# Optimization experiments

Hardware: AMD Instinct MI355X
Metric: run time of the kernel (lower is better)

## Reference

```python
import jax, jax.numpy as jnp
import numpy as np

LN_EPS = 1e-5

def setup_inputs() -> dict:
    key = jax.random.key(0)
    ks = jax.random.split(key, 6)
    B, H, W, C = 32, 128, 96, 128
    ch = C // 2
    x = jax.random.normal(ks[0], (B, H, W, C), dtype=jnp.float32)
    # he_normal-style scaled init for 1x1 conv kernels (fan_in = C or ch)
    wq_ch = jax.random.normal(ks[1], (C,), dtype=jnp.float32) * np.float32(np.sqrt(2.0 / C))
    wv_ch = jax.random.normal(ks[2], (C, ch), dtype=jnp.float32) * np.float32(np.sqrt(2.0 / C))
    w_ch = jax.random.normal(ks[3], (ch, C), dtype=jnp.float32) * np.float32(np.sqrt(2.0 / ch))
    gamma = jnp.ones((C,), dtype=jnp.float32)
    beta = jnp.zeros((C,), dtype=jnp.float32)
    wq_sp = jax.random.normal(ks[4], (C, ch), dtype=jnp.float32) * np.float32(np.sqrt(2.0 / C))
    wv_sp = jax.random.normal(ks[5], (C, ch), dtype=jnp.float32) * np.float32(np.sqrt(2.0 / C))
    return {"x": x, "wq_ch": wq_ch, "wv_ch": wv_ch, "w_ch": w_ch,
            "gamma": gamma, "beta": beta, "wq_sp": wq_sp, "wv_sp": wv_sp}


def reference(x, wq_ch, wv_ch, w_ch, gamma, beta, wq_sp, wv_sp):
    B, H, W, C = x.shape
    hw = H * W
    ch = C // 2

    # ---- channel-only self-attention ----
    # q: 1x1 conv C->1, flatten to [B, HW], softmax over spatial positions
    q = jnp.einsum('bhwc,c->bhw', x, wq_ch).reshape(B, hw)
    q = jax.nn.softmax(q, axis=-1)
    # v: 1x1 conv C->C/2, flatten to [B, HW, C/2]
    v = jnp.einsum('bhwc,cd->bhwd', x, wv_ch).reshape(B, hw, ch)
    ctx = jnp.einsum('bn,bnd->bd', q, v)          # [B, C/2]
    ctx = ctx @ w_ch                               # 1x1 conv C/2 -> C, [B, C]
    # LayerNorm over axes [1,2,3] of (B,1,1,C) == per-sample norm over C
    mu = jnp.mean(ctx, axis=-1, keepdims=True)
    var = jnp.mean(jnp.square(ctx - mu), axis=-1, keepdims=True)
    ctx = (ctx - mu) * jax.lax.rsqrt(var + LN_EPS) * gamma + beta
    mask_ch = jax.nn.sigmoid(ctx)                  # [B, C]
    ch_out = x * mask_ch[:, None, None, :]

    # ---- spatial-only self-attention (parallel mode: input is x) ----
    # 1x1 conv C->C/2 followed by global avg pool == avg-pooled x projected
    q_sp = jnp.einsum('bhwc,cd->bd', x, wq_sp) / hw  # [B, C/2]
    q_sp = jax.nn.softmax(q_sp, axis=-1)
    v_sp = jnp.einsum('bhwc,cd->bhwd', x, wv_sp).reshape(B, hw, ch)
    sp_ctx = jnp.einsum('bd,bnd->bn', q_sp, v_sp).reshape(B, H, W, 1)
    sp_out = x * jax.nn.sigmoid(sp_ctx)

    return ch_out + sp_out
```

## Files before the change

### kernel.cpp

```cpp
#include <hip/hip_runtime.h>

#define BSZ 32
#define CC  128
#define CH  64
#define HWN 12288
#define BPB 64
#define ROWS (HWN/BPB)

using f4 = __attribute__((ext_vector_type(4))) float;

__global__ __launch_bounds__(256) void psa_pass1(
    const float* __restrict__ x, const float* __restrict__ wq_ch,
    float* __restrict__ pS, float* __restrict__ pX, float* __restrict__ pZ)
{
    const int b    = blockIdx.x / BPB;
    const int blk  = blockIdx.x % BPB;
    const int tid  = threadIdx.x;
    const int l32  = tid & 31;
    const int slot = tid >> 5;

    const f4 wq = reinterpret_cast<const f4*>(wq_ch)[l32];

    float s0=0.f,s1=0.f,s2=0.f,s3=0.f;
    float a0=0.f,a1=0.f,a2=0.f,a3=0.f;
    float zacc=0.f;

    const float* xb = x + (size_t)b * (size_t)(HWN * CC);
    const int row0 = blk * ROWS;

    for (int i = slot; i < ROWS; i += 32) {
        const f4 x0 = reinterpret_cast<const f4*>(xb + (size_t)(row0 + i)      * CC)[l32];
        const f4 x1 = reinterpret_cast<const f4*>(xb + (size_t)(row0 + i + 8)  * CC)[l32];
        const f4 x2 = reinterpret_cast<const f4*>(xb + (size_t)(row0 + i + 16) * CC)[l32];
        const f4 x3 = reinterpret_cast<const f4*>(xb + (size_t)(row0 + i + 24) * CC)[l32];
        float p0 = x0.x*wq.x + x0.y*wq.y + x0.z*wq.z + x0.w*wq.w;
        float p1 = x1.x*wq.x + x1.y*wq.y + x1.z*wq.z + x1.w*wq.w;
        float p2 = x2.x*wq.x + x2.y*wq.y + x2.z*wq.z + x2.w*wq.w;
        float p3 = x3.x*wq.x + x3.y*wq.y + x3.z*wq.z + x3.w*wq.w;
        p0 += __shfl_xor(p0, 1);  p1 += __shfl_xor(p1, 1);
        p2 += __shfl_xor(p2, 1);  p3 += __shfl_xor(p3, 1);
        p0 += __shfl_xor(p0, 2);  p1 += __shfl_xor(p1, 2);
        p2 += __shfl_xor(p2, 2);  p3 += __shfl_xor(p3, 2);
        p0 += __shfl_xor(p0, 4);  p1 += __shfl_xor(p1, 4);
        p2 += __shfl_xor(p2, 4);  p3 += __shfl_xor(p3, 4);
        p0 += __shfl_xor(p0, 8);  p1 += __shfl_xor(p1, 8);
        p2 += __shfl_xor(p2, 8);  p3 += __shfl_xor(p3, 8);
        p0 += __shfl_xor(p0, 16); p1 += __shfl_xor(p1, 16);
        p2 += __shfl_xor(p2, 16); p3 += __shfl_xor(p3, 16);
        const float e0 = __expf(p0), e1 = __expf(p1);
        const float e2 = __expf(p2), e3 = __expf(p3);
        if (l32 == 0) zacc += (e0 + e1) + (e2 + e3);
        s0 += e0*x0.x + e1*x1.x + e2*x2.x + e3*x3.x;
        s1 += e0*x0.y + e1*x1.y + e2*x2.y + e3*x3.y;
        s2 += e0*x0.z + e1*x1.z + e2*x2.z + e3*x3.z;
        s3 += e0*x0.w + e1*x1.w + e2*x2.w + e3*x3.w;
        a0 += (x0.x + x1.x) + (x2.x + x3.x);
        a1 += (x0.y + x1.y) + (x2.y + x3.y);
        a2 += (x0.z + x1.z) + (x2.z + x3.z);
        a3 += (x0.w + x1.w) + (x2.w + x3.w);
    }

    __shared__ float Ssh[CC];
    __shared__ float Xsh[CC];
    __shared__ float zsh;
    if (tid < CC) { Ssh[tid] = 0.f; Xsh[tid] = 0.f; }
    if (tid == 0) zsh = 0.f;
    __syncthreads();

    const int cb = l32 * 4;
    atomicAdd(&Ssh[cb+0], s0); atomicAdd(&Ssh[cb+1], s1);
    atomicAdd(&Ssh[cb+2], s2); atomicAdd(&Ssh[cb+3], s3);
    atomicAdd(&Xsh[cb+0], a0); atomicAdd(&Xsh[cb+1], a1);
    atomicAdd(&Xsh[cb+2], a2); atomicAdd(&Xsh[cb+3], a3);
    if (l32 == 0) atomicAdd(&zsh, zacc);
    __syncthreads();

    const size_t base = (size_t)(b * BPB + blk) * CC;
    if (tid < CC) {
        pS[base + tid] = Ssh[tid];
        pX[base + tid] = Xsh[tid];
    }
    if (tid == 0) pZ[b * BPB + blk] = zsh;
}

__global__ __launch_bounds__(128) void psa_mid(
    const float* __restrict__ pS, const float* __restrict__ pX,
    const float* __restrict__ pZ,
    const float* __restrict__ wv_ch, const float* __restrict__ w_ch,
    const float* __restrict__ gamma, const float* __restrict__ beta,
    const float* __restrict__ wq_sp, const float* __restrict__ wv_sp,
    float* __restrict__ mask_ch, float* __restrict__ wf)
{
    const int b = blockIdx.x;
    const int t = threadIdx.x;

    __shared__ float Ssh[CC], Xsh[CC], ctxh[CH], qsp[CH], zsh, red2[2];

    {
        const float* pSb = pS + (size_t)b * BPB * CC;
        const float* pXb = pX + (size_t)b * BPB * CC;
        float s = 0.f, a = 0.f;
        #pragma unroll
        for (int k = 0; k < BPB; ++k) {
            s += pSb[(size_t)k * CC + t];
            a += pXb[(size_t)k * CC + t];
        }
        Ssh[t] = s; Xsh[t] = a;
    }
    if (t < 64) {
        float z = pZ[b * BPB + t];
        z += __shfl_xor(z, 1); z += __shfl_xor(z, 2);  z += __shfl_xor(z, 4);
        z += __shfl_xor(z, 8); z += __shfl_xor(z, 16); z += __shfl_xor(z, 32);
        if (t == 0) zsh = z;
    }
    __syncthreads();

    if (t < CH) {
        float a = 0.f, aq = 0.f;
        #pragma unroll
        for (int c = 0; c < CC; ++c) {
            a  += Ssh[c] * wv_ch[c*CH + t];
            aq += Xsh[c] * wq_sp[c*CH + t];
        }
        ctxh[t] = a / zsh;
        float q = aq * (1.0f / (float)HWN);
        float m = q;
        m = fmaxf(m, __shfl_xor(m, 1));  m = fmaxf(m, __shfl_xor(m, 2));
        m = fmaxf(m, __shfl_xor(m, 4));  m = fmaxf(m, __shfl_xor(m, 8));
        m = fmaxf(m, __shfl_xor(m, 16)); m = fmaxf(m, __shfl_xor(m, 32));
        float e = __expf(q - m);
        float sum = e;
        sum += __shfl_xor(sum, 1);  sum += __shfl_xor(sum, 2);
        sum += __shfl_xor(sum, 4);  sum += __shfl_xor(sum, 8);
        sum += __shfl_xor(sum, 16); sum += __shfl_xor(sum, 32);
        qsp[t] = e / sum;
    }
    __syncthreads();

    float ctx = 0.f;
    #pragma unroll
    for (int d = 0; d < CH; ++d) ctx += ctxh[d] * w_ch[d*CC + t];

    const int wid = t >> 6;
    {
        float r = ctx;
        r += __shfl_xor(r, 1);  r += __shfl_xor(r, 2);  r += __shfl_xor(r, 4);
        r += __shfl_xor(r, 8);  r += __shfl_xor(r, 16); r += __shfl_xor(r, 32);
        if ((t & 63) == 0) red2[wid] = r;
    }
    __syncthreads();
    const float mu = (red2[0] + red2[1]) * (1.0f / CC);
    __syncthreads();
    const float dc = ctx - mu;
    {
        float r = dc * dc;
        r += __shfl_xor(r, 1);  r += __shfl_xor(r, 2);  r += __shfl_xor(r, 4);
        r += __shfl_xor(r, 8);  r += __shfl_xor(r, 16); r += __shfl_xor(r, 32);
        if ((t & 63) == 0) red2[wid] = r;
    }
    __syncthreads();
    const float var = (red2[0] + red2[1]) * (1.0f / CC);

    const float nrm = dc * rsqrtf(var + 1e-5f) * gamma[t] + beta[t];
    mask_ch[b*CC + t] = 1.0f / (1.0f + __expf(-nrm));

    float wacc = 0.f;
    #pragma unroll
    for (int d = 0; d < CH; ++d) wacc += wv_sp[t*CH + d] * qsp[d];
    wf[b*CC + t] = wacc;
}

__global__ __launch_bounds__(256) void psa_pass2(
    const float* __restrict__ x, const float* __restrict__ mask_ch,
    const float* __restrict__ wf, float* __restrict__ out)
{
    const int b    = blockIdx.x / BPB;
    const int blk  = blockIdx.x % BPB;
    const int tid  = threadIdx.x;
    const int l32  = tid & 31;
    const int slot = tid >> 5;

    const f4 m4 = reinterpret_cast<const f4*>(mask_ch + b*CC)[l32];
    const f4 w4 = reinterpret_cast<const f4*>(wf + b*CC)[l32];

    const float* xb = x   + (size_t)b * (size_t)(HWN * CC);
    float*       ob = out + (size_t)b * (size_t)(HWN * CC);
    const int row0 = blk * ROWS;

    for (int i = slot; i < ROWS; i += 32) {
        const size_t off0 = (size_t)(row0 + i)      * CC;
        const size_t off1 = (size_t)(row0 + i + 8)  * CC;
        const size_t off2 = (size_t)(row0 + i + 16) * CC;
        const size_t off3 = (size_t)(row0 + i + 24) * CC;
        const f4 x0 = reinterpret_cast<const f4*>(xb + off0)[l32];
        const f4 x1 = reinterpret_cast<const f4*>(xb + off1)[l32];
        const f4 x2 = reinterpret_cast<const f4*>(xb + off2)[l32];
        const f4 x3 = reinterpret_cast<const f4*>(xb + off3)[l32];
        float p0 = x0.x*w4.x + x0.y*w4.y + x0.z*w4.z + x0.w*w4.w;
        float p1 = x1.x*w4.x + x1.y*w4.y + x1.z*w4.z + x1.w*w4.w;
        float p2 = x2.x*w4.x + x2.y*w4.y + x2.z*w4.z + x2.w*w4.w;
        float p3 = x3.x*w4.x + x3.y*w4.y + x3.z*w4.z + x3.w*w4.w;
        p0 += __shfl_xor(p0, 1);  p1 += __shfl_xor(p1, 1);
        p2 += __shfl_xor(p2, 1);  p3 += __shfl_xor(p3, 1);
        p0 += __shfl_xor(p0, 2);  p1 += __shfl_xor(p1, 2);
        p2 += __shfl_xor(p2, 2);  p3 += __shfl_xor(p3, 2);
        p0 += __shfl_xor(p0, 4);  p1 += __shfl_xor(p1, 4);
        p2 += __shfl_xor(p2, 4);  p3 += __shfl_xor(p3, 4);
        p0 += __shfl_xor(p0, 8);  p1 += __shfl_xor(p1, 8);
        p2 += __shfl_xor(p2, 8);  p3 += __shfl_xor(p3, 8);
        p0 += __shfl_xor(p0, 16); p1 += __shfl_xor(p1, 16);
        p2 += __shfl_xor(p2, 16); p3 += __shfl_xor(p3, 16);
        const float g0 = 1.0f / (1.0f + __expf(-p0));
        const float g1 = 1.0f / (1.0f + __expf(-p1));
        const float g2 = 1.0f / (1.0f + __expf(-p2));
        const float g3 = 1.0f / (1.0f + __expf(-p3));
        f4 o0, o1, o2, o3;
        o0.x = x0.x*(m4.x+g0); o0.y = x0.y*(m4.y+g0); o0.z = x0.z*(m4.z+g0); o0.w = x0.w*(m4.w+g0);
        o1.x = x1.x*(m4.x+g1); o1.y = x1.y*(m4.y+g1); o1.z = x1.z*(m4.z+g1); o1.w = x1.w*(m4.w+g1);
        o2.x = x2.x*(m4.x+g2); o2.y = x2.y*(m4.y+g2); o2.z = x2.z*(m4.z+g2); o2.w = x2.w*(m4.w+g2);
        o3.x = x3.x*(m4.x+g3); o3.y = x3.y*(m4.y+g3); o3.z = x3.z*(m4.z+g3); o3.w = x3.w*(m4.w+g3);
        __builtin_nontemporal_store(o0, reinterpret_cast<f4*>(ob + off0) + l32);
        __builtin_nontemporal_store(o1, reinterpret_cast<f4*>(ob + off1) + l32);
        __builtin_nontemporal_store(o2, reinterpret_cast<f4*>(ob + off2) + l32);
        __builtin_nontemporal_store(o3, reinterpret_cast<f4*>(ob + off3) + l32);
    }
}

extern "C" void kernel_launch(void* const* d_in, const int* in_sizes, int n_in,
                              void* d_out, int out_size, void* d_ws, size_t ws_size,
                              hipStream_t stream) {
    const float* x     = (const float*)d_in[0];
    const float* wq_ch = (const float*)d_in[1];
    const float* wv_ch = (const float*)d_in[2];
    const float* w_ch  = (const float*)d_in[3];
    const float* gamma = (const float*)d_in[4];
    const float* beta  = (const float*)d_in[5];
    const float* wq_sp = (const float*)d_in[6];
    const float* wv_sp = (const float*)d_in[7];
    float* out = (float*)d_out;

    float* ws   = (float*)d_ws;
    float* pS   = ws;
    float* pX   = pS + (size_t)BSZ*BPB*CC;
    float* pZ   = pX + (size_t)BSZ*BPB*CC;
    float* mask = pZ + BSZ*BPB;
    float* wf   = mask + BSZ*CC;

    psa_pass1<<<BSZ*BPB, 256, 0, stream>>>(x, wq_ch, pS, pX, pZ);
    psa_mid  <<<BSZ,     128, 0, stream>>>(pS, pX, pZ, wv_ch, w_ch, gamma, beta,
                                           wq_sp, wv_sp, mask, wf);
    psa_pass2<<<BSZ*BPB, 256, 0, stream>>>(x, mask, wf, out);
}
```

Before: 118.6 us.

## Fold per-sample mid kernel into pass2 blocks, removing one launch

The small per-batch mid kernel, which reduces partial sums and computes the channel mask and spatial weight vector, is removed. Each pass2 block now recomputes that per-sample work redundantly in shared memory before streaming x. This drops a kernel launch and the low-parallelism 32-block serial stage between the two bandwidth-bound passes. In exchange, every one of the 64 blocks per sample re-reads the partials (64x128x2 floats) and the weights and repeats the small GEMVs. Launch bounds also gain an occupancy hint of 8.

```diff
diff --git a/kernel.cpp b/kernel.cpp
--- a/kernel.cpp
+++ b/kernel.cpp
@@ -9,7 +9,7 @@
 
 using f4 = __attribute__((ext_vector_type(4))) float;
 
-__global__ __launch_bounds__(256) void psa_pass1(
+__global__ __launch_bounds__(256, 8) void psa_pass1(
     const float* __restrict__ x, const float* __restrict__ wq_ch,
     float* __restrict__ pS, float* __restrict__ pX, float* __restrict__ pZ)
 {
@@ -83,46 +83,52 @@
     if (tid == 0) pZ[b * BPB + blk] = zsh;
 }
 
-__global__ __launch_bounds__(128) void psa_mid(
+__global__ __launch_bounds__(256, 8) void psa_pass2(
+    const float* __restrict__ x,
     const float* __restrict__ pS, const float* __restrict__ pX,
     const float* __restrict__ pZ,
     const float* __restrict__ wv_ch, const float* __restrict__ w_ch,
     const float* __restrict__ gamma, const float* __restrict__ beta,
     const float* __restrict__ wq_sp, const float* __restrict__ wv_sp,
-    float* __restrict__ mask_ch, float* __restrict__ wf)
+    float* __restrict__ out)
 {
-    const int b = blockIdx.x;
-    const int t = threadIdx.x;
-
-    __shared__ float Ssh[CC], Xsh[CC], ctxh[CH], qsp[CH], zsh, red2[2];
-
-    {
+    const int b    = blockIdx.x / BPB;
+    const int blk  = blockIdx.x % BPB;
+    const int tid  = threadIdx.x;
+    const int l32  = tid & 31;
+    const int slot = tid >> 5;
+
+    __shared__ float Ssh[CC], Xsh[CC], ctxh[CH], qsp[CH];
+    __shared__ __align__(16) float mask_sh[CC], wf_sh[CC];
+    __shared__ float zsh, red2[2];
+
+    if (tid < CC) {
         const float* pSb = pS + (size_t)b * BPB * CC;
         const float* pXb = pX + (size_t)b * BPB * CC;
         float s = 0.f, a = 0.f;
         #pragma unroll
         for (int k = 0; k < BPB; ++k) {
-            s += pSb[(size_t)k * CC + t];
-            a += pXb[(size_t)k * CC + t];
+            s += pSb[(size_t)k * CC + tid];
+            a += pXb[(size_t)k * CC + tid];
         }
-        Ssh[t] = s; Xsh[t] = a;
-    }
-    if (t < 64) {
-        float z = pZ[b * BPB + t];
+        Ssh[tid] = s; Xsh[tid] = a;
+    }
+    if (tid < 64) {
+        float z = pZ[b * BPB + tid];
         z += __shfl_xor(z, 1); z += __shfl_xor(z, 2);  z += __shfl_xor(z, 4);
         z += __shfl_xor(z, 8); z += __shfl_xor(z, 16); z += __shfl_xor(z, 32);
-        if (t == 0) zsh = z;
-    }
-    __syncthreads();
-
-    if (t < CH) {
+        if (tid == 0) zsh = z;
+    }
+    __syncthreads();
+
+    if (tid < CH) {
         float a = 0.f, aq = 0.f;
         #pragma unroll
         for (int c = 0; c < CC; ++c) {
-            a  += Ssh[c] * wv_ch[c*CH + t];
-            aq += Xsh[c] * wq_sp[c*CH + t];
+            a  += Ssh[c] * wv_ch[c*CH + tid];
+            aq += Xsh[c] * wq_sp[c*CH + tid];
         }
-        ctxh[t] = a / zsh;
+        ctxh[tid] = a / zsh;
         float q = aq * (1.0f / (float)HWN);
         float m = q;
         m = fmaxf(m, __shfl_xor(m, 1));  m = fmaxf(m, __shfl_xor(m, 2));
@@ -133,55 +139,46 @@
         sum += __shfl_xor(sum, 1);  sum += __shfl_xor(sum, 2);
         sum += __shfl_xor(sum, 4);  sum += __shfl_xor(sum, 8);
         sum += __shfl_xor(sum, 16); sum += __shfl_xor(sum, 32);
-        qsp[t] = e / sum;
+        qsp[tid] = e / sum;
     }
     __syncthreads();
 
     float ctx = 0.f;
-    #pragma unroll
-    for (int d = 0; d < CH; ++d) ctx += ctxh[d] * w_ch[d*CC + t];
-
-    const int wid = t >> 6;
+    if (tid < CC) {
+        #pragma unroll
+        for (int d = 0; d < CH; ++d) ctx += ctxh[d] * w_ch[d*CC + tid];
+    }
     {
-        float r = ctx;
+        float r = (tid < CC) ? ctx : 0.f;
         r += __shfl_xor(r, 1);  r += __shfl_xor(r, 2);  r += __shfl_xor(r, 4);
         r += __shfl_xor(r, 8);  r += __shfl_xor(r, 16); r += __shfl_xor(r, 32);
-        if ((t & 63) == 0) red2[wid] = r;
+        if ((tid & 63) == 0 && tid < CC) red2[tid >> 6] = r;
     }
     __syncthreads();
     const float mu = (red2[0] + red2[1]) * (1.0f / CC);
     __syncthreads();
-    const float dc = ctx - mu;
+    const float dc = (tid < CC) ? (ctx - mu) : 0.f;
     {
         float r = dc * dc;
         r += __shfl_xor(r, 1);  r += __shfl_xor(r, 2);  r += __shfl_xor(r, 4);
         r += __shfl_xor(r, 8);  r += __shfl_xor(r, 16); r += __shfl_xor(r, 32);
-        if ((t & 63) == 0) red2[wid] = r;
+        if ((tid & 63) == 0 && tid < CC) red2[tid >> 6] = r;
     }
     __syncthreads();
     const float var = (red2[0] + red2[1]) * (1.0f / CC);
 
-    const float nrm = dc * rsqrtf(var + 1e-5f) * gamma[t] + beta[t];
-    mask_ch[b*CC + t] = 1.0f / (1.0f + __expf(-nrm));
-
-    float wacc = 0.f;
-    #pragma unroll
-    for (int d = 0; d < CH; ++d) wacc += wv_sp[t*CH + d] * qsp[d];
-    wf[b*CC + t] = wacc;
-}
-
-__global__ __launch_bounds__(256) void psa_pass2(
-    const float* __restrict__ x, const float* __restrict__ mask_ch,
-    const float* __restrict__ wf, float* __restrict__ out)
-{
-    const int b    = blockIdx.x / BPB;
-    const int blk  = blockIdx.x % BPB;
-    const int tid  = threadIdx.x;
-    const int l32  = tid & 31;
-    const int slot = tid >> 5;
-
-    const f4 m4 = reinterpret_cast<const f4*>(mask_ch + b*CC)[l32];
-    const f4 w4 = reinterpret_cast<const f4*>(wf + b*CC)[l32];
+    if (tid < CC) {
+        const float nrm = dc * rsqrtf(var + 1e-5f) * gamma[tid] + beta[tid];
+        mask_sh[tid] = 1.0f / (1.0f + __expf(-nrm));
+        float wacc = 0.f;
+        #pragma unroll
+        for (int d = 0; d < CH; ++d) wacc += wv_sp[tid*CH + d] * qsp[d];
+        wf_sh[tid] = wacc;
+    }
+    __syncthreads();
+
+    const f4 m4 = reinterpret_cast<const f4*>(mask_sh)[l32];
+    const f4 w4 = reinterpret_cast<const f4*>(wf_sh)[l32];
 
     const float* xb = x   + (size_t)b * (size_t)(HWN * CC);
     float*       ob = out + (size_t)b * (size_t)(HWN * CC);
@@ -239,15 +236,12 @@
     const float* wv_sp = (const float*)d_in[7];
     float* out = (float*)d_out;
 
-    float* ws   = (float*)d_ws;
-    float* pS   = ws;
-    float* pX   = pS + (size_t)BSZ*BPB*CC;
-    float* pZ   = pX + (size_t)BSZ*BPB*CC;
-    float* mask = pZ + BSZ*BPB;
-    float* wf   = mask + BSZ*CC;
+    float* ws = (float*)d_ws;
+    float* pS = ws;
+    float* pX = pS + (size_t)BSZ*BPB*CC;
+    float* pZ = pX + (size_t)BSZ*BPB*CC;
 
     psa_pass1<<<BSZ*BPB, 256, 0, stream>>>(x, wq_ch, pS, pX, pZ);
-    psa_mid  <<<BSZ,     128, 0, stream>>>(pS, pX, pZ, wv_ch, w_ch, gamma, beta,
-                                           wq_sp, wv_sp, mask, wf);
-    psa_pass2<<<BSZ*BPB, 256, 0, stream>>>(x, mask, wf, out);
+    psa_pass2<<<BSZ*BPB, 256, 0, stream>>>(x, pS, pX, pZ, wv_ch, w_ch,
+                                           gamma, beta, wq_sp, wv_sp, out);
 }
```

After: 122.5 us. 1.03x slower.
